# Kernel tuning notes

Measured on AMD Instinct MI355X. Metric: run time of the kernel, lower is better.

Reference implementation:

```python
import jax, jax.numpy as jnp
import numpy as np

H = 1024      # hidden_dim
NH = 16       # num_heads
HD = H // NH  # head_dim
FF = 4096     # ff_dim
EPS = 1e-6


def layer_norm(x, gamma, beta):
    # faithful to source: unbiased std (ddof=1), divide by (std + eps)
    mean = jnp.mean(x, axis=-1, keepdims=True)
    var = jnp.sum((x - mean) ** 2, axis=-1, keepdims=True) / (x.shape[-1] - 1)
    std = jnp.sqrt(var)
    return gamma * (x - mean) / (std + EPS) + beta


def linear_mulbias(x, W, b):
    # source LinearLayer: einsum('...i,io,o->...o') -> (x @ W) * b (bias MULTIPLIES)
    return jnp.einsum('bti,io->bto', x, W) * b


def setup_inputs() -> dict:
    key = jax.random.key(0)
    ks = jax.random.split(key, 11)
    B, T = 2, 2048
    return {
        'x':      jax.random.normal(ks[0], (B, T, H), jnp.float32),
        'Wqkv':   jax.random.normal(ks[1], (H, 3 * H), jnp.float32),
        'bqkv':   jax.random.normal(ks[2], (3 * H,), jnp.float32),
        'W1':     jax.random.normal(ks[3], (H, FF), jnp.float32),
        'b1':     jax.random.normal(ks[4], (FF,), jnp.float32),
        'W2':     jax.random.normal(ks[5], (FF, H), jnp.float32),
        'b2':     jax.random.normal(ks[6], (H,), jnp.float32),
        'gamma1': jax.random.normal(ks[7], (H,), jnp.float32),
        'beta1':  jax.random.normal(ks[8], (H,), jnp.float32),
        'gamma2': jax.random.normal(ks[9], (H,), jnp.float32),
        'beta2':  jax.random.normal(ks[10], (H,), jnp.float32),
    }


def attention(x, Wqkv, bqkv):
    B, T, _ = x.shape
    qkv = linear_mulbias(x, Wqkv, bqkv)                 # [B,T,3H]
    # einops 'b t (d k h) -> k b h t d' with k=3, h=NH: last dim decomposes (d,3,h)
    qkv = qkv.reshape(B, T, HD, 3, NH)
    qkv = jnp.transpose(qkv, (3, 0, 4, 1, 2))           # [3,B,NH,T,HD]
    q, k, v = qkv[0], qkv[1], qkv[2]
    scores = jnp.einsum('bhid,bhjd->bhij', q, k) / (H ** 0.5)  # scale by full hidden_dim
    attn = jax.nn.softmax(scores, axis=-1)
    out = jnp.einsum('bhij,bhjd->bhid', attn, v)        # [B,NH,T,HD]
    return jnp.transpose(out, (0, 2, 1, 3)).reshape(B, T, H)


def reference(x, Wqkv, bqkv, W1, b1, W2, b2, gamma1, beta1, gamma2, beta2):
    # dropout is identity in eval mode
    out = layer_norm(x + attention(x, Wqkv, bqkv), gamma1, beta1)
    ffn = linear_mulbias(jnp.maximum(linear_mulbias(out, W1, b1), 0.0), W2, b2)
    out = layer_norm(out + ffn, gamma2, beta2)
    return out
```

## Files before the change

### kernel.cpp

```cpp
#include <hip/hip_runtime.h>
#include <math.h>

#define B 2
#define T 2048
#define H 1024
#define NH 16
#define HD 64
#define FF 4096
#define M_TOK (B*T)
#define LOG2E 1.4426950408889634f

typedef unsigned short u16;
typedef __attribute__((ext_vector_type(8))) short bf16x8;
typedef __attribute__((ext_vector_type(4))) float f32x4;

#define WAITBAR3  asm volatile("s_waitcnt vmcnt(3)\n\ts_barrier" ::: "memory")
#define WAITBAR4  asm volatile("s_waitcnt vmcnt(4)\n\ts_barrier" ::: "memory")
#define WAITBAR0  asm volatile("s_waitcnt vmcnt(0)\n\ts_barrier" ::: "memory")

__device__ __forceinline__ u16 f2bf(float f) {
  union { float f; unsigned u; } v; v.f = f;
  const unsigned r = (v.u + 0x7FFFu + ((v.u >> 16) & 1u)) >> 16;
  return (u16)r;
}
__device__ __forceinline__ float bf2f(u16 h) {
  union { unsigned u; float f; } v; v.u = ((unsigned)h) << 16;
  return v.f;
}
__device__ __forceinline__ unsigned cvt_pk_bf16(float lo, float hi) {
  unsigned r;
  asm("v_cvt_pk_bf16_f32 %0, %1, %2" : "=v"(r) : "v"(lo), "v"(hi));
  return r;
}
__device__ __forceinline__ float m3(float a, float b, float c) {
  return fmaxf(fmaxf(a, b), c);
}
__device__ __forceinline__ void gload16(const u16* g, u16* l) {
  __builtin_amdgcn_global_load_lds(
      (const __attribute__((address_space(1))) unsigned int*)g,
      (__attribute__((address_space(3))) unsigned int*)l, 16, 0, 0);
}

__global__ __launch_bounds__(256) void preprocess(
    const float* __restrict__ x, u16* __restrict__ xh, u16* __restrict__ xl,
    const float* __restrict__ Wqkv, u16* __restrict__ WqTh, u16* __restrict__ WqTl,
    const float* __restrict__ W1_, u16* __restrict__ W1T_,
    const float* __restrict__ W2_, u16* __restrict__ W2T_)
{
  const int bid = blockIdx.x;
  const int tid = threadIdx.x;
  if (bid < 4096) {
    const size_t i = ((size_t)bid * 256 + tid) * 4;
    const float4 v = *(const float4*)(x + i);
    union { u16 s[4]; uint2 u; } h, l;
    const float f[4] = {v.x, v.y, v.z, v.w};
#pragma unroll
    for (int j = 0; j < 4; ++j) {
      const u16 hb = f2bf(f[j]); h.s[j] = hb; l.s[j] = f2bf(f[j] - bf2f(hb));
    }
    *(uint2*)(xh + i) = h.u;
    *(uint2*)(xl + i) = l.u;
    return;
  }
  __shared__ float tile[64][69];
  const float* in; u16* oh; u16* ol = nullptr; int K, N, k0, n0, split = 0;
  if (bid < 4864) {
    const int tb = bid - 4096;
    in = Wqkv; oh = WqTh; ol = WqTl; K = H; N = 3*H; split = 1;
    n0 = (tb % 48) * 64; k0 = (tb / 48) * 64;
  } else if (bid < 5888) {
    const int tb = bid - 4864;
    in = W1_; oh = W1T_; K = H; N = FF;
    n0 = (tb & 63) * 64; k0 = (tb >> 6) * 64;
  } else {
    const int tb = bid - 5888;
    in = W2_; oh = W2T_; K = FF; N = H;
    n0 = (tb & 15) * 64; k0 = (tb >> 4) * 64;
  }
  const int r = tid >> 4, c4 = (tid & 15) * 4;
#pragma unroll
  for (int i = 0; i < 4; ++i) {
    const float4 v = *(const float4*)(in + (size_t)(k0 + i*16 + r) * N + n0 + c4);
    tile[i*16+r][c4]   = v.x; tile[i*16+r][c4+1] = v.y;
    tile[i*16+r][c4+2] = v.z; tile[i*16+r][c4+3] = v.w;
  }
  __syncthreads();
  const int n = tid >> 2, kq = tid & 3;
  union { u16 s[8]; int4 v; } ph0, ph1, pl0, pl1;
#pragma unroll
  for (int j = 0; j < 8; ++j) {
    const float f0 = tile[kq*16 + j][n];
    const float f1 = tile[kq*16 + 8 + j][n];
    const u16 h0 = f2bf(f0), h1 = f2bf(f1);
    ph0.s[j] = h0; ph1.s[j] = h1;
    if (split) { pl0.s[j] = f2bf(f0 - bf2f(h0)); pl1.s[j] = f2bf(f1 - bf2f(h1)); }
  }
  u16* po = oh + (size_t)(n0 + n) * K + k0 + kq * 16;
  *(int4*)po = ph0.v; *(int4*)(po + 8) = ph1.v;
  if (split) {
    u16* pl = ol + (size_t)(n0 + n) * K + k0 + kq * 16;
    *(int4*)pl = pl0.v; *(int4*)(pl + 8) = pl1.v;
  }
}

__device__ __forceinline__ int swz(int r, int kq) {
  return r * 32 + ((kq ^ ((r >> 1) & 3)) * 8);
}

template<int SPLIT, int RELU, int OBF, int QKV3, int DEEP3>
__global__ __launch_bounds__(256) void mfma_gemm(
    const u16* __restrict__ Ah, const u16* __restrict__ Al,
    const u16* __restrict__ Bh, const u16* __restrict__ Bl,
    const float* __restrict__ bias,
    float* __restrict__ Cf, u16* __restrict__ Cb,
    int M, int N, int K)
{
  __shared__ u16 lds[DEEP3 ? 24576 : (SPLIT ? 32768 : 16384)];
  const int BUFSZ = SPLIT ? 16384 : 8192;
  const int tid = threadIdx.x;
  const int bid = blockIdx.x;
  const int xcd = bid & 7;
  const int idx = bid >> 3;
  const int row0 = (xcd * 4 + (idx & 3)) * 128;
  const int col0 = (idx >> 2) * 128;
  const int wv = tid >> 6, lane = tid & 63;
  const int wr = wv >> 1, wc = wv & 1;
  const int kq = lane >> 4, fr = lane & 15;

  f32x4 acc[4][4] = {};

#define GSTAGE(lbase, gb, rowbase, kk) do { \
    _Pragma("unroll") \
    for (int t_ = 0; t_ < 2; ++t_) { \
      const int c_ = wv * 2 + t_; \
      const int idx_ = c_ * 64 + lane; \
      const int r_ = idx_ >> 2; \
      const int kq_ = (idx_ & 3) ^ ((r_ >> 1) & 3); \
      gload16((gb) + (size_t)((rowbase) + r_) * K + (kk) + kq_ * 8, \
              &lds[(lbase) + c_ * 512]); \
    } } while (0)

#define BLSTAGE(lbase, kk) do { \
    _Pragma("unroll") \
    for (int t_ = 0; t_ < 2; ++t_) { \
      const int c_ = wv * 2 + t_; \
      if (!QKV3 || ((((col0 >> 4) + c_) % 3) != 2)) { \
        const int idx_ = c_ * 64 + lane; \
        const int r_ = idx_ >> 2; \
        const int kq_ = (idx_ & 3) ^ ((r_ >> 1) & 3); \
        gload16(Bl + (size_t)(col0 + r_) * K + (kk) + kq_ * 8, \
                &lds[(lbase) + c_ * 512]); \
      } } } while (0)

  if (DEEP3) {
    const int nk = K >> 5;
    GSTAGE(0, Ah, row0, 0);            GSTAGE(4096, Bh, col0, 0);
    GSTAGE(8192, Ah, row0, 32);        GSTAGE(8192 + 4096, Bh, col0, 32);
    WAITBAR4;
    int cslot = 0, islot = 2;
    for (int i = 0; i < nk; ++i) {
      if (i + 2 < nk) {
        const int kk = (i + 2) * 32;
        GSTAGE(islot * 8192, Ah, row0, kk);
        GSTAGE(islot * 8192 + 4096, Bh, col0, kk);
        islot = (islot == 2) ? 0 : islot + 1;
      }
      const int rb = cslot * 8192;
      bf16x8 a_h[4];
#pragma unroll
      for (int m = 0; m < 4; ++m)
        a_h[m] = *(const bf16x8*)&lds[rb + swz(wr*64 + m*16 + fr, kq)];
#pragma unroll
      for (int n = 0; n < 4; ++n) {
        const bf16x8 b_h = *(const bf16x8*)&lds[rb + 4096 + swz(wc*64 + n*16 + fr, kq)];
#pragma unroll
        for (int m = 0; m < 4; ++m)
          acc[m][n] = __builtin_amdgcn_mfma_f32_16x16x32_bf16(a_h[m], b_h, acc[m][n], 0, 0, 0);
      }
      cslot = (cslot == 2) ? 0 : cslot + 1;
      if (i + 1 < nk) { if (i + 2 < nk) WAITBAR4; else WAITBAR0; }
    }
  } else {
    GSTAGE(0, Ah, row0, 0);
    GSTAGE(4096, Bh, col0, 0);
    if (SPLIT) { GSTAGE(8192, Al, row0, 0); BLSTAGE(12288, 0); }
    __syncthreads();

    int cur = 0;
    for (int k0 = 0; k0 < K; k0 += 32) {
      const int nxt = cur ^ 1;
      if (k0 + 32 < K) {
        GSTAGE(nxt*BUFSZ, Ah, row0, k0 + 32);
        GSTAGE(nxt*BUFSZ + 4096, Bh, col0, k0 + 32);
        if (SPLIT) { GSTAGE(nxt*BUFSZ + 8192, Al, row0, k0 + 32);
                     BLSTAGE(nxt*BUFSZ + 12288, k0 + 32); }
      }
      const int rb = cur * BUFSZ;
      bf16x8 a_h[4], a_l[4];
#pragma unroll
      for (int m = 0; m < 4; ++m) {
        a_h[m] = *(const bf16x8*)&lds[rb + swz(wr*64 + m*16 + fr, kq)];
        if (SPLIT) a_l[m] = *(const bf16x8*)&lds[rb + 8192 + swz(wr*64 + m*16 + fr, kq)];
      }
#pragma unroll
      for (int n = 0; n < 4; ++n) {
        const bf16x8 b_h = *(const bf16x8*)&lds[rb + 4096 + swz(wc*64 + n*16 + fr, kq)];
#pragma unroll
        for (int m = 0; m < 4; ++m)
          acc[m][n] = __builtin_amdgcn_mfma_f32_16x16x32_bf16(a_h[m], b_h, acc[m][n], 0, 0, 0);
        if (SPLIT) {
          const bool dolo = !QKV3 || ((((col0 >> 4) + wc * 4 + n) % 3) != 2);
          if (dolo) {
            const bf16x8 b_l = *(const bf16x8*)&lds[rb + 12288 + swz(wc*64 + n*16 + fr, kq)];
#pragma unroll
            for (int m = 0; m < 4; ++m) {
              acc[m][n] = __builtin_amdgcn_mfma_f32_16x16x32_bf16(a_h[m], b_l, acc[m][n], 0, 0, 0);
              acc[m][n] = __builtin_amdgcn_mfma_f32_16x16x32_bf16(a_l[m], b_h, acc[m][n], 0, 0, 0);
            }
          }
        }
      }
      __syncthreads();
      cur = nxt;
    }
  }
#undef GSTAGE
#undef BLSTAGE

  const int orow0 = row0 + wr * 64, ocol0 = col0 + wc * 64;
#pragma unroll
  for (int n = 0; n < 4; ++n) {
    const int col = ocol0 + n * 16 + fr;
    const float bs = bias[col];
#pragma unroll
    for (int m = 0; m < 4; ++m) {
      const int rbase = orow0 + m * 16 + (lane >> 4) * 4;
#pragma unroll
      for (int j = 0; j < 4; ++j) {
        float v = acc[m][n][j] * bs;
        if (RELU) v = fmaxf(v, 0.0f);
        const size_t off = (size_t)(rbase + j) * N + col;
        if (OBF) Cb[off] = f2bf(v); else Cf[off] = v;
      }
    }
  }
}

__global__ __launch_bounds__(512, 2) void mfma_ffn2(
    const u16* __restrict__ Ah, const u16* __restrict__ Bh,
    const u16* __restrict__ Res, const float* __restrict__ bias,
    float* __restrict__ Y)
{
  const int N = H, K = FF;
  __shared__ u16 lds[2 * 24576];
  const int tid = threadIdx.x;
  const int bid = blockIdx.x;
  const int xcd = bid & 7;
  const int idx = bid >> 3;
  const int row0 = (xcd * 4 + (idx & 3)) * 128;
  const int col0 = (idx >> 2) * 128;
  const int wv8 = tid >> 6, lane = tid & 63;
  const int grp = wv8 >> 2, wv = wv8 & 3;
  const int wr = wv >> 1, wc = wv & 1;
  const int kq = lane >> 4, fr = lane & 15;
  const int kb = grp * (K >> 1);
  u16* gl = &lds[grp * 24576];

  f32x4 acc[4][4] = {};

#define GSTAGE2(lbase, gb, rowbase, kk) do { \
    _Pragma("unroll") \
    for (int t_ = 0; t_ < 2; ++t_) { \
      const int c_ = wv * 2 + t_; \
      const int idx_ = c_ * 64 + lane; \
      const int r_ = idx_ >> 2; \
      const int kq_ = (idx_ & 3) ^ ((r_ >> 1) & 3); \
      gload16((gb) + (size_t)((rowbase) + r_) * K + (kk) + kq_ * 8, \
              &gl[(lbase) + c_ * 512]); \
    } } while (0)

  const int nk = (K >> 1) >> 5;
  GSTAGE2(0, Ah, row0, kb);            GSTAGE2(4096, Bh, col0, kb);
  GSTAGE2(8192, Ah, row0, kb + 32);    GSTAGE2(8192 + 4096, Bh, col0, kb + 32);
  WAITBAR4;
  int cslot = 0, islot = 2;
  for (int i = 0; i < nk; ++i) {
    if (i + 2 < nk) {
      const int kk = kb + (i + 2) * 32;
      GSTAGE2(islot * 8192, Ah, row0, kk);
      GSTAGE2(islot * 8192 + 4096, Bh, col0, kk);
      islot = (islot == 2) ? 0 : islot + 1;
    }
    const int rb = cslot * 8192;
    bf16x8 a_h[4];
#pragma unroll
    for (int m = 0; m < 4; ++m)
      a_h[m] = *(const bf16x8*)&gl[rb + swz(wr*64 + m*16 + fr, kq)];
#pragma unroll
    for (int n = 0; n < 4; ++n) {
      const bf16x8 b_h = *(const bf16x8*)&gl[rb + 4096 + swz(wc*64 + n*16 + fr, kq)];
#pragma unroll
      for (int m = 0; m < 4; ++m)
        acc[m][n] = __builtin_amdgcn_mfma_f32_16x16x32_bf16(a_h[m], b_h, acc[m][n], 0, 0, 0);
    }
    cslot = (cslot == 2) ? 0 : cslot + 1;
    if (i + 1 < nk) { if (i + 2 < nk) WAITBAR4; else WAITBAR0; }
  }
#undef GSTAGE2

  __syncthreads();
  float* fm = (float*)lds;
  const int base = wv * 4096;
  if (grp == 1) {
#pragma unroll
    for (int m = 0; m < 4; ++m)
#pragma unroll
      for (int n = 0; n < 4; ++n)
        *(f32x4*)&fm[base + (m*4 + n)*256 + lane*4] = acc[m][n];
  }
  __syncthreads();
  if (grp == 0) {
    const int orow0 = row0 + wr * 64, ocol0 = col0 + wc * 64;
#pragma unroll
    for (int n = 0; n < 4; ++n) {
      const int col = ocol0 + n * 16 + fr;
      const float bs = bias[col];
#pragma unroll
      for (int m = 0; m < 4; ++m) {
        const f32x4 ob = *(const f32x4*)&fm[base + (m*4 + n)*256 + lane*4];
        const int rbase = orow0 + m * 16 + kq * 4;
#pragma unroll
        for (int j = 0; j < 4; ++j) {
          const size_t off = (size_t)(rbase + j) * N + col;
          Y[off] = bf2f(Res[off]) + (acc[m][n][j] + ob[j]) * bs;
        }
      }
    }
  }
}

__device__ __forceinline__ int padi(int o) { return o + 4 * (o >> 6); }

__global__ __launch_bounds__(256) void repack_qkv(
    const float* __restrict__ qkv,
    u16* __restrict__ Qh, u16* __restrict__ Ql,
    u16* __restrict__ Kh, u16* __restrict__ Kl, u16* __restrict__ Vb)
{
  const int bt = blockIdx.x;
  const int b = bt >> 11, t = bt & (T - 1);
  const int tid = threadIdx.x;
  __shared__ float Ls[3 * H + 192];
  const float* src = qkv + (size_t)bt * (3 * H);
#pragma unroll
  for (int i = 0; i < 3; ++i) {
    const int o = (i * 256 + tid) * 4;
    *(float4*)&Ls[padi(o)] = *(const float4*)(src + o);
  }
  __syncthreads();
  const float qscale = LOG2E / 32.0f;
  const int h = tid >> 4, d0 = (tid & 15) * 4;
  const size_t dst = (((size_t)(b * NH + h)) * T + t) * HD + d0;
  union { u16 s[4]; uint2 u; } qh_, ql_, kh_, kl_, vb_;
#pragma unroll
  for (int jj = 0; jj < 4; ++jj) {
    const int ob = (d0 + jj) * 48 + h;
    const float q = Ls[padi(ob)] * qscale;
    const float k = Ls[padi(ob + 16)];
    const float v = Ls[padi(ob + 32)];
    const u16 qhb = f2bf(q);
    qh_.s[jj] = qhb; ql_.s[jj] = f2bf(q - bf2f(qhb));
    const u16 khb = f2bf(k);
    kh_.s[jj] = khb; kl_.s[jj] = f2bf(k - bf2f(khb));
    vb_.s[jj] = f2bf(v);
  }
  *(uint2*)(Qh + dst) = qh_.u;
  *(uint2*)(Ql + dst) = ql_.u;
  *(uint2*)(Kh + dst) = kh_.u;
  *(uint2*)(Kl + dst) = kl_.u;
  *(uint2*)(Vb + dst) = vb_.u;
}

__global__ __launch_bounds__(256) void vtrans(
    const u16* __restrict__ Vb, u16* __restrict__ VT)
{
  __shared__ u16 Ls[64][72];
  const int bh = blockIdx.y, t0 = blockIdx.x * 64;
  const int tid = threadIdx.x;
  const int r = tid >> 2, c = (tid & 3) * 16;
  const size_t src = ((size_t)bh * T + t0 + r) * HD + c;
  *(int4*)&Ls[r][c]     = *(const int4*)(Vb + src);
  *(int4*)&Ls[r][c + 8] = *(const int4*)(Vb + src + 8);
  __syncthreads();
  const int d = tid >> 2, tc = (tid & 3) * 16;
  u16 buf[16];
#pragma unroll
  for (int i = 0; i < 16; ++i) buf[i] = Ls[tc + i][d];
  u16* dst = VT + ((size_t)bh * HD + d) * T + t0 + tc;
  *(int4*)dst       = *(int4*)&buf[0];
  *(int4*)(dst + 8) = *(int4*)&buf[8];
}

__device__ __forceinline__ int sigma_k(int r) {
  return ((r >> 5) << 5) | (((r >> 2) & 3) << 3) | (((r >> 4) & 1) << 2) | (r & 3);
}

__global__ __launch_bounds__(512, 4) void flash_attn_mfma(
    const u16* __restrict__ Qh, const u16* __restrict__ Ql,
    const u16* __restrict__ Kh, const u16* __restrict__ Kl,
    const u16* __restrict__ VT, float* __restrict__ Out)
{
  __shared__ u16 sm[3 * 12288];
  const int i = blockIdx.x;
  const int slot = i >> 3;
  const int bh = (i & 7) * 4 + (slot >> 4);
  const int row0 = (slot & 15) * 128;
  const int b = bh >> 4, h = bh & 15;
  const int tid = threadIdx.x, wave = tid >> 6, lane = tid & 63;
  const int fr = lane & 15, kq = lane >> 4;

  bf16x8 qh[2], ql[2];
  const size_t qoff = ((size_t)bh * T + row0 + wave*16 + fr) * HD + kq*8;
#pragma unroll
  for (int ks = 0; ks < 2; ++ks) {
    qh[ks] = *(const bf16x8*)(Qh + qoff + ks*32);
    ql[ks] = *(const bf16x8*)(Ql + qoff + ks*32);
  }

  bf16x8 ones8;
#pragma unroll
  for (int z = 0; z < 8; ++z) ones8[z] = (short)0x3F80;

  f32x4 o[4] = {};
  f32x4 oex = {};
  float m_ = -1e30f;

  const int c_ = wave;
  const int r0_ = c_ * 8 + (lane >> 3), s_ = lane & 7;
  const int cd0 = s_ ^ (r0_ & 7);
  const int k0_ = sigma_k(r0_);
  const u16* pKh0 = Kh + ((size_t)bh*T + k0_)*HD + cd0*8;
  const u16* pKl0 = Kl + ((size_t)bh*T + k0_)*HD + cd0*8;
  const u16* pV0  = VT + ((size_t)bh*HD + r0_)*T + cd0*8;

#define FSTAGE(sb) do { \
    gload16(pKh0, &sm[(sb) + c_*512]); \
    gload16(pKl0, &sm[(sb) + 4096 + c_*512]); \
    gload16(pV0,  &sm[(sb) + 8192 + c_*512]); \
    pKh0 += 64*HD; pKl0 += 64*HD; pV0 += 64; \
  } while (0)

  FSTAGE(0);
  FSTAGE(12288);
  WAITBAR3;
  int cslot = 0, islot = 2;

  const int NT = T / 64;
  for (int t = 0; t < NT; ++t) {
    if (t + 2 < NT) {
      FSTAGE(islot * 12288);
      islot = (islot == 2) ? 0 : islot + 1;
    }
    const u16* smb = &sm[cslot * 12288];

    f32x4 s[4] = {};
    __builtin_amdgcn_s_setprio(1);
#pragma unroll
    for (int ks = 0; ks < 2; ++ks) {
#pragma unroll
      for (int n = 0; n < 4; ++n) {
        const int kr = n * 16 + fr;
        const int sl = ((ks*4 + kq) ^ (kr & 7)) * 8;
        const bf16x8 kh_ = *(const bf16x8*)&smb[kr*64 + sl];
        const bf16x8 kl_ = *(const bf16x8*)&smb[4096 + kr*64 + sl];
        s[n] = __builtin_amdgcn_mfma_f32_16x16x32_bf16(kh_, qh[ks], s[n], 0, 0, 0);
        s[n] = __builtin_amdgcn_mfma_f32_16x16x32_bf16(kl_, qh[ks], s[n], 0, 0, 0);
        s[n] = __builtin_amdgcn_mfma_f32_16x16x32_bf16(kh_, ql[ks], s[n], 0, 0, 0);
      }
    }
    __builtin_amdgcn_s_setprio(0);

    const float g0 = m3(s[0][0], s[0][1], s[0][2]);
    const float g1 = m3(s[0][3], s[1][0], s[1][1]);
    const float g2 = m3(s[1][2], s[1][3], s[2][0]);
    const float g3 = m3(s[2][1], s[2][2], s[2][3]);
    const float g4 = m3(s[3][0], s[3][1], s[3][2]);
    float mx = fmaxf(m3(g0, g1, g2), m3(g3, g4, s[3][3]));
    mx = fmaxf(mx, __shfl_xor(mx, 16));
    mx = fmaxf(mx, __shfl_xor(mx, 32));
    if (!__all(mx <= m_ + 8.0f)) {
      const float mn = fmaxf(m_, mx);
      const float fsc = exp2f(m_ - mn);
      m_ = mn;
#pragma unroll
      for (int n = 0; n < 4; ++n) {
        o[n][0] *= fsc; o[n][1] *= fsc;
        o[n][2] *= fsc; o[n][3] *= fsc;
      }
      oex[0] *= fsc; oex[1] *= fsc; oex[2] *= fsc; oex[3] *= fsc;
    }

    float p[4][4];
#pragma unroll
    for (int n = 0; n < 4; ++n)
#pragma unroll
      for (int jj = 0; jj < 4; ++jj)
        p[n][jj] = exp2f(s[n][jj] - m_);

    unsigned pk[4][2];
#pragma unroll
    for (int n = 0; n < 4; ++n) {
      pk[n][0] = cvt_pk_bf16(p[n][0], p[n][1]);
      pk[n][1] = cvt_pk_bf16(p[n][2], p[n][3]);
    }

    __builtin_amdgcn_s_setprio(1);
#pragma unroll
    for (int ks = 0; ks < 2; ++ks) {
      union { unsigned u[4]; bf16x8 v; } pb;
      pb.u[0] = pk[2*ks][0];   pb.u[1] = pk[2*ks][1];
      pb.u[2] = pk[2*ks+1][0]; pb.u[3] = pk[2*ks+1][1];
#pragma unroll
      for (int n = 0; n < 4; ++n) {
        const int dr = n * 16 + fr;
        const bf16x8 vf = *(const bf16x8*)&smb[8192 + dr*64 + (((ks*4 + kq) ^ (dr & 7)) * 8)];
        o[n] = __builtin_amdgcn_mfma_f32_16x16x32_bf16(vf, pb.v, o[n], 0, 0, 0);
      }
      oex = __builtin_amdgcn_mfma_f32_16x16x32_bf16(ones8, pb.v, oex, 0, 0, 0);
    }
    __builtin_amdgcn_s_setprio(0);

    cslot = (cslot == 2) ? 0 : cslot + 1;
    if (t + 1 < NT) { if (t + 2 < NT) WAITBAR3; else WAITBAR0; }
  }
#undef FSTAGE

  {
    const float inv = 1.0f / oex[0];
    const size_t qrow = (size_t)b * T + row0 + wave*16 + fr;
#pragma unroll
    for (int n = 0; n < 4; ++n) {
      float4 ov;
      ov.x = o[n][0] * inv; ov.y = o[n][1] * inv;
      ov.z = o[n][2] * inv; ov.w = o[n][3] * inv;
      *(float4*)(Out + qrow * H + h * HD + n * 16 + kq * 4) = ov;
    }
  }
}

__global__ __launch_bounds__(256) void ln_residual(
    const float* __restrict__ A, const float* __restrict__ Bz,
    const float* __restrict__ gamma, const float* __restrict__ beta,
    u16* __restrict__ obf)
{
  const int row = blockIdx.x, tid = threadIdx.x;
  const int wave = tid >> 6, lane = tid & 63;
  const size_t off = (size_t)row * H + tid * 4;
  const float4 av = *(const float4*)(A + off);
  const float4 bv = *(const float4*)(Bz + off);
  float4 y; y.x = av.x + bv.x; y.y = av.y + bv.y; y.z = av.z + bv.z; y.w = av.w + bv.w;
  float s  = y.x + y.y + y.z + y.w;
  float ss = y.x*y.x + y.y*y.y + y.z*y.z + y.w*y.w;
#pragma unroll
  for (int o = 32; o >= 1; o >>= 1) { s += __shfl_xor(s, o); ss += __shfl_xor(ss, o); }
  __shared__ float red[2][4];
  if (lane == 0) { red[0][wave] = s; red[1][wave] = ss; }
  __syncthreads();
  s  = red[0][0] + red[0][1] + red[0][2] + red[0][3];
  ss = red[1][0] + red[1][1] + red[1][2] + red[1][3];
  const float mean = s * (1.0f / (float)H);
  float var = (ss - (float)H * mean * mean) * (1.0f / (float)(H - 1));
  var = fmaxf(var, 0.0f);
  const float inv = 1.0f / (sqrtf(var) + 1e-6f);
  const float4 gv = *(const float4*)(gamma + tid * 4);
  const float4 be = *(const float4*)(beta + tid * 4);
  float4 o;
  o.x = gv.x * (y.x - mean) * inv + be.x;
  o.y = gv.y * (y.y - mean) * inv + be.y;
  o.z = gv.z * (y.z - mean) * inv + be.z;
  o.w = gv.w * (y.w - mean) * inv + be.w;
  union { u16 s[4]; uint2 u; } pk;
  pk.s[0] = f2bf(o.x); pk.s[1] = f2bf(o.y); pk.s[2] = f2bf(o.z); pk.s[3] = f2bf(o.w);
  *(uint2*)(obf + off) = pk.u;
}

__global__ __launch_bounds__(256) void ln_only(
    const float* __restrict__ Yv,
    const float* __restrict__ gamma, const float* __restrict__ beta,
    float* __restrict__ out)
{
  const int row = blockIdx.x, tid = threadIdx.x;
  const int wave = tid >> 6, lane = tid & 63;
  const size_t off = (size_t)row * H + tid * 4;
  const float4 y = *(const float4*)(Yv + off);
  float s  = y.x + y.y + y.z + y.w;
  float ss = y.x*y.x + y.y*y.y + y.z*y.z + y.w*y.w;
#pragma unroll
  for (int o = 32; o >= 1; o >>= 1) { s += __shfl_xor(s, o); ss += __shfl_xor(ss, o); }
  __shared__ float red[2][4];
  if (lane == 0) { red[0][wave] = s; red[1][wave] = ss; }
  __syncthreads();
  s  = red[0][0] + red[0][1] + red[0][2] + red[0][3];
  ss = red[1][0] + red[1][1] + red[1][2] + red[1][3];
  const float mean = s * (1.0f / (float)H);
  float var = (ss - (float)H * mean * mean) * (1.0f / (float)(H - 1));
  var = fmaxf(var, 0.0f);
  const float inv = 1.0f / (sqrtf(var) + 1e-6f);
  const float4 gv = *(const float4*)(gamma + tid * 4);
  const float4 be = *(const float4*)(beta + tid * 4);
  float4 o;
  o.x = gv.x * (y.x - mean) * inv + be.x;
  o.y = gv.y * (y.y - mean) * inv + be.y;
  o.z = gv.z * (y.z - mean) * inv + be.z;
  o.w = gv.w * (y.w - mean) * inv + be.w;
  *(float4*)(out + off) = o;
}

extern "C" void kernel_launch(void* const* d_in, const int* in_sizes, int n_in,
                              void* d_out, int out_size, void* d_ws, size_t ws_size,
                              hipStream_t stream)
{
  const float* x    = (const float*)d_in[0];
  const float* Wqkv = (const float*)d_in[1];
  const float* bqkv = (const float*)d_in[2];
  const float* W1   = (const float*)d_in[3];
  const float* b1   = (const float*)d_in[4];
  const float* W2   = (const float*)d_in[5];
  const float* b2   = (const float*)d_in[6];
  const float* g1   = (const float*)d_in[7];
  const float* be1  = (const float*)d_in[8];
  const float* g2   = (const float*)d_in[9];
  const float* be2  = (const float*)d_in[10];
  float* out = (float*)d_out;
  char* w = (char*)d_ws;

  float* qkv  = (float*)(w + 0);
  u16*   h1b  = (u16*)  (w + 0);
  u16*   xh   = (u16*)  (w + 52428800);
  u16*   xl   = (u16*)  (w + 60817408);
  u16*   Qh   = (u16*)  (w + 52428800);
  u16*   Ql   = (u16*)  (w + 60817408);
  u16*   WqTh = (u16*)  (w + 69206016);
  u16*   WqTl = (u16*)  (w + 75497472);
  u16*   Khb  = (u16*)  (w + 69206016);
  u16*   Klb  = (u16*)  (w + 77594624);
  u16*   Vbb  = (u16*)  (w + 85983232);
  u16*   VTb  = (u16*)  (w + 94371840);
  float* attn = (float*)(w + 102760448);
  float* Yb   = (float*)(w + 102760448);
  u16*   W1T  = (u16*)  (w + 119537664);
  u16*   W2T  = (u16*)  (w + 127926272);
  u16*   ln1b = (u16*)  (w + 136314880);

  preprocess<<<6912, 256, 0, stream>>>(x, xh, xl, Wqkv, WqTh, WqTl,
                                       W1, W1T, W2, W2T);
  mfma_gemm<1,0,0,1,0><<<24 * 32, 256, 0, stream>>>(xh, xl, WqTh, WqTl, bqkv,
                                                    qkv, nullptr, M_TOK, 3*H, H);
  repack_qkv<<<M_TOK, 256, 0, stream>>>(qkv, Qh, Ql, Khb, Klb, Vbb);
  vtrans<<<dim3(T/64, B*NH), 256, 0, stream>>>(Vbb, VTb);
  flash_attn_mfma<<<512, 512, 0, stream>>>(Qh, Ql, Khb, Klb, VTb, attn);
  ln_residual<<<M_TOK, 256, 0, stream>>>(x, attn, g1, be1, ln1b);
  mfma_gemm<0,1,1,0,1><<<32 * 32, 256, 0, stream>>>(ln1b, nullptr, W1T, nullptr, b1,
                                                    nullptr, h1b, M_TOK, FF, H);
  mfma_ffn2<<<256, 512, 0, stream>>>(h1b, W2T, ln1b, b2, Yb);
  ln_only<<<M_TOK, 256, 0, stream>>>(Yb, g2, be2, out);
}
```

Measured before the change: 292.2 us.

## Fuse QKV repack into QKV GEMM epilogue via permuted weight columns

Permutes the Wqkv columns (and the bias) during preprocessing so the QKV GEMM output columns come out grouped as Q, K, V by head and dim. A dedicated QKV GEMM kernel then writes bf16 hi/lo Q, K and V directly in head-major layout, which removes the fp32 qkv intermediate and the separate repack kernel. It also picks the split-precision path per block (V blocks skip the low parts) instead of per fragment. The epilogue writes are scattered 2-byte stores, which could be less efficient than the old coalesced repack.

After: 268.3 us. 8.2% less time.

```diff
diff --git a/kernel.cpp b/kernel.cpp
--- a/kernel.cpp
+++ b/kernel.cpp
@@ -41,14 +41,29 @@
       (__attribute__((address_space(3))) unsigned int*)l, 16, 0, 0);
 }
 
+__device__ __forceinline__ int colperm(int c) {
+  const int d = c / 48;
+  const int rem = c - d * 48;
+  return ((rem >> 4) << 10) | ((rem & 15) << 6) | d;
+}
+
 __global__ __launch_bounds__(256) void preprocess(
     const float* __restrict__ x, u16* __restrict__ xh, u16* __restrict__ xl,
     const float* __restrict__ Wqkv, u16* __restrict__ WqTh, u16* __restrict__ WqTl,
     const float* __restrict__ W1_, u16* __restrict__ W1T_,
-    const float* __restrict__ W2_, u16* __restrict__ W2T_)
+    const float* __restrict__ W2_, u16* __restrict__ W2T_,
+    const float* __restrict__ bqkv, float* __restrict__ bqkvP)
 {
   const int bid = blockIdx.x;
   const int tid = threadIdx.x;
+  if (bid == 6912) {
+#pragma unroll
+    for (int it = 0; it < 12; ++it) {
+      const int c = it * 256 + tid;
+      bqkvP[colperm(c)] = bqkv[c];
+    }
+    return;
+  }
   if (bid < 4096) {
     const size_t i = ((size_t)bid * 256 + tid) * 4;
     const float4 v = *(const float4*)(x + i);
@@ -63,10 +78,11 @@
     return;
   }
   __shared__ float tile[64][69];
-  const float* in; u16* oh; u16* ol = nullptr; int K, N, k0, n0, split = 0;
+  const float* in; u16* oh; u16* ol = nullptr;
+  int K, N, k0, n0, split = 0, permq = 0;
   if (bid < 4864) {
     const int tb = bid - 4096;
-    in = Wqkv; oh = WqTh; ol = WqTl; K = H; N = 3*H; split = 1;
+    in = Wqkv; oh = WqTh; ol = WqTl; K = H; N = 3*H; split = 1; permq = 1;
     n0 = (tb % 48) * 64; k0 = (tb / 48) * 64;
   } else if (bid < 5888) {
     const int tb = bid - 4864;
@@ -95,10 +111,12 @@
     ph0.s[j] = h0; ph1.s[j] = h1;
     if (split) { pl0.s[j] = f2bf(f0 - bf2f(h0)); pl1.s[j] = f2bf(f1 - bf2f(h1)); }
   }
-  u16* po = oh + (size_t)(n0 + n) * K + k0 + kq * 16;
+  int orow = n0 + n;
+  if (permq) orow = colperm(orow);
+  u16* po = oh + (size_t)orow * K + k0 + kq * 16;
   *(int4*)po = ph0.v; *(int4*)(po + 8) = ph1.v;
   if (split) {
-    u16* pl = ol + (size_t)(n0 + n) * K + k0 + kq * 16;
+    u16* pl = ol + (size_t)orow * K + k0 + kq * 16;
     *(int4*)pl = pl0.v; *(int4*)(pl + 8) = pl1.v;
   }
 }
@@ -107,16 +125,14 @@
   return r * 32 + ((kq ^ ((r >> 1) & 3)) * 8);
 }
 
-template<int SPLIT, int RELU, int OBF, int QKV3, int DEEP3>
+template<int RELU, int OBF>
 __global__ __launch_bounds__(256) void mfma_gemm(
-    const u16* __restrict__ Ah, const u16* __restrict__ Al,
-    const u16* __restrict__ Bh, const u16* __restrict__ Bl,
+    const u16* __restrict__ Ah, const u16* __restrict__ Bh,
     const float* __restrict__ bias,
     float* __restrict__ Cf, u16* __restrict__ Cb,
     int M, int N, int K)
 {
-  __shared__ u16 lds[DEEP3 ? 24576 : (SPLIT ? 32768 : 16384)];
-  const int BUFSZ = SPLIT ? 16384 : 8192;
+  __shared__ u16 lds[24576];
   const int tid = threadIdx.x;
   const int bid = blockIdx.x;
   const int xcd = bid & 7;
@@ -140,92 +156,34 @@
               &lds[(lbase) + c_ * 512]); \
     } } while (0)
 
-#define BLSTAGE(lbase, kk) do { \
-    _Pragma("unroll") \
-    for (int t_ = 0; t_ < 2; ++t_) { \
-      const int c_ = wv * 2 + t_; \
-      if (!QKV3 || ((((col0 >> 4) + c_) % 3) != 2)) { \
-        const int idx_ = c_ * 64 + lane; \
-        const int r_ = idx_ >> 2; \
-        const int kq_ = (idx_ & 3) ^ ((r_ >> 1) & 3); \
-        gload16(Bl + (size_t)(col0 + r_) * K + (kk) + kq_ * 8, \
-                &lds[(lbase) + c_ * 512]); \
-      } } } while (0)
-
-  if (DEEP3) {
-    const int nk = K >> 5;
-    GSTAGE(0, Ah, row0, 0);            GSTAGE(4096, Bh, col0, 0);
-    GSTAGE(8192, Ah, row0, 32);        GSTAGE(8192 + 4096, Bh, col0, 32);
-    WAITBAR4;
-    int cslot = 0, islot = 2;
-    for (int i = 0; i < nk; ++i) {
-      if (i + 2 < nk) {
-        const int kk = (i + 2) * 32;
-        GSTAGE(islot * 8192, Ah, row0, kk);
-        GSTAGE(islot * 8192 + 4096, Bh, col0, kk);
-        islot = (islot == 2) ? 0 : islot + 1;
-      }
-      const int rb = cslot * 8192;
-      bf16x8 a_h[4];
+  const int nk = K >> 5;
+  GSTAGE(0, Ah, row0, 0);            GSTAGE(4096, Bh, col0, 0);
+  GSTAGE(8192, Ah, row0, 32);        GSTAGE(8192 + 4096, Bh, col0, 32);
+  WAITBAR4;
+  int cslot = 0, islot = 2;
+  for (int i = 0; i < nk; ++i) {
+    if (i + 2 < nk) {
+      const int kk = (i + 2) * 32;
+      GSTAGE(islot * 8192, Ah, row0, kk);
+      GSTAGE(islot * 8192 + 4096, Bh, col0, kk);
+      islot = (islot == 2) ? 0 : islot + 1;
+    }
+    const int rb = cslot * 8192;
+    bf16x8 a_h[4];
+#pragma unroll
+    for (int m = 0; m < 4; ++m)
+      a_h[m] = *(const bf16x8*)&lds[rb + swz(wr*64 + m*16 + fr, kq)];
+#pragma unroll
+    for (int n = 0; n < 4; ++n) {
+      const bf16x8 b_h = *(const bf16x8*)&lds[rb + 4096 + swz(wc*64 + n*16 + fr, kq)];
 #pragma unroll
       for (int m = 0; m < 4; ++m)
-        a_h[m] = *(const bf16x8*)&lds[rb + swz(wr*64 + m*16 + fr, kq)];
-#pragma unroll
-      for (int n = 0; n < 4; ++n) {
-        const bf16x8 b_h = *(const bf16x8*)&lds[rb + 4096 + swz(wc*64 + n*16 + fr, kq)];
-#pragma unroll
-        for (int m = 0; m < 4; ++m)
-          acc[m][n] = __builtin_amdgcn_mfma_f32_16x16x32_bf16(a_h[m], b_h, acc[m][n], 0, 0, 0);
-      }
-      cslot = (cslot == 2) ? 0 : cslot + 1;
-      if (i + 1 < nk) { if (i + 2 < nk) WAITBAR4; else WAITBAR0; }
-    }
-  } else {
-    GSTAGE(0, Ah, row0, 0);
-    GSTAGE(4096, Bh, col0, 0);
-    if (SPLIT) { GSTAGE(8192, Al, row0, 0); BLSTAGE(12288, 0); }
-    __syncthreads();
-
-    int cur = 0;
-    for (int k0 = 0; k0 < K; k0 += 32) {
-      const int nxt = cur ^ 1;
-      if (k0 + 32 < K) {
-        GSTAGE(nxt*BUFSZ, Ah, row0, k0 + 32);
-        GSTAGE(nxt*BUFSZ + 4096, Bh, col0, k0 + 32);
-        if (SPLIT) { GSTAGE(nxt*BUFSZ + 8192, Al, row0, k0 + 32);
-                     BLSTAGE(nxt*BUFSZ + 12288, k0 + 32); }
-      }
-      const int rb = cur * BUFSZ;
-      bf16x8 a_h[4], a_l[4];
-#pragma unroll
-      for (int m = 0; m < 4; ++m) {
-        a_h[m] = *(const bf16x8*)&lds[rb + swz(wr*64 + m*16 + fr, kq)];
-        if (SPLIT) a_l[m] = *(const bf16x8*)&lds[rb + 8192 + swz(wr*64 + m*16 + fr, kq)];
-      }
-#pragma unroll
-      for (int n = 0; n < 4; ++n) {
-        const bf16x8 b_h = *(const bf16x8*)&lds[rb + 4096 + swz(wc*64 + n*16 + fr, kq)];
-#pragma unroll
-        for (int m = 0; m < 4; ++m)
-          acc[m][n] = __builtin_amdgcn_mfma_f32_16x16x32_bf16(a_h[m], b_h, acc[m][n], 0, 0, 0);
-        if (SPLIT) {
-          const bool dolo = !QKV3 || ((((col0 >> 4) + wc * 4 + n) % 3) != 2);
-          if (dolo) {
-            const bf16x8 b_l = *(const bf16x8*)&lds[rb + 12288 + swz(wc*64 + n*16 + fr, kq)];
-#pragma unroll
-            for (int m = 0; m < 4; ++m) {
-              acc[m][n] = __builtin_amdgcn_mfma_f32_16x16x32_bf16(a_h[m], b_l, acc[m][n], 0, 0, 0);
-              acc[m][n] = __builtin_amdgcn_mfma_f32_16x16x32_bf16(a_l[m], b_h, acc[m][n], 0, 0, 0);
-            }
-          }
-        }
-      }
-      __syncthreads();
-      cur = nxt;
-    }
+        acc[m][n] = __builtin_amdgcn_mfma_f32_16x16x32_bf16(a_h[m], b_h, acc[m][n], 0, 0, 0);
+    }
+    cslot = (cslot == 2) ? 0 : cslot + 1;
+    if (i + 1 < nk) { if (i + 2 < nk) WAITBAR4; else WAITBAR0; }
   }
 #undef GSTAGE
-#undef BLSTAGE
 
   const int orow0 = row0 + wr * 64, ocol0 = col0 + wc * 64;
 #pragma unroll
@@ -234,13 +192,119 @@
     const float bs = bias[col];
 #pragma unroll
     for (int m = 0; m < 4; ++m) {
-      const int rbase = orow0 + m * 16 + (lane >> 4) * 4;
+      const int rbase = orow0 + m * 16 + kq * 4;
 #pragma unroll
       for (int j = 0; j < 4; ++j) {
         float v = acc[m][n][j] * bs;
         if (RELU) v = fmaxf(v, 0.0f);
         const size_t off = (size_t)(rbase + j) * N + col;
         if (OBF) Cb[off] = f2bf(v); else Cf[off] = v;
+      }
+    }
+  }
+}
+
+__global__ __launch_bounds__(256) void mfma_qkv(
+    const u16* __restrict__ Ah, const u16* __restrict__ Al,
+    const u16* __restrict__ Bh, const u16* __restrict__ Bl,
+    const float* __restrict__ biasP,
+    u16* __restrict__ Qh, u16* __restrict__ Ql,
+    u16* __restrict__ Kh, u16* __restrict__ Kl, u16* __restrict__ Vb)
+{
+  const int K = H;
+  __shared__ u16 lds[32768];
+  const int tid = threadIdx.x;
+  const int bid = blockIdx.x;
+  const int xcd = bid & 7;
+  const int idx = bid >> 3;
+  const int row0 = (xcd * 4 + (idx & 3)) * 128;
+  const int col0 = (idx >> 2) * 128;
+  const int wv = tid >> 6, lane = tid & 63;
+  const int wr = wv >> 1, wc = wv & 1;
+  const int kq = lane >> 4, fr = lane & 15;
+  const bool isV = (col0 >= 2048);
+
+  f32x4 acc[4][4] = {};
+
+#define QSTAGE(lbase, gb, rowbase, kk) do { \
+    _Pragma("unroll") \
+    for (int t_ = 0; t_ < 2; ++t_) { \
+      const int c_ = wv * 2 + t_; \
+      const int idx_ = c_ * 64 + lane; \
+      const int r_ = idx_ >> 2; \
+      const int kq_ = (idx_ & 3) ^ ((r_ >> 1) & 3); \
+      gload16((gb) + (size_t)((rowbase) + r_) * K + (kk) + kq_ * 8, \
+              &lds[(lbase) + c_ * 512]); \
+    } } while (0)
+
+  QSTAGE(0, Ah, row0, 0);
+  QSTAGE(4096, Bh, col0, 0);
+  if (!isV) { QSTAGE(8192, Al, row0, 0); QSTAGE(12288, Bl, col0, 0); }
+  __syncthreads();
+
+  int cur = 0;
+  for (int k0 = 0; k0 < K; k0 += 32) {
+    const int nxt = cur ^ 1;
+    if (k0 + 32 < K) {
+      QSTAGE(nxt*16384, Ah, row0, k0 + 32);
+      QSTAGE(nxt*16384 + 4096, Bh, col0, k0 + 32);
+      if (!isV) { QSTAGE(nxt*16384 + 8192, Al, row0, k0 + 32);
+                  QSTAGE(nxt*16384 + 12288, Bl, col0, k0 + 32); }
+    }
+    const int rb = cur * 16384;
+    bf16x8 a_h[4], a_l[4];
+#pragma unroll
+    for (int m = 0; m < 4; ++m) {
+      a_h[m] = *(const bf16x8*)&lds[rb + swz(wr*64 + m*16 + fr, kq)];
+      if (!isV) a_l[m] = *(const bf16x8*)&lds[rb + 8192 + swz(wr*64 + m*16 + fr, kq)];
+    }
+#pragma unroll
+    for (int n = 0; n < 4; ++n) {
+      const bf16x8 b_h = *(const bf16x8*)&lds[rb + 4096 + swz(wc*64 + n*16 + fr, kq)];
+#pragma unroll
+      for (int m = 0; m < 4; ++m)
+        acc[m][n] = __builtin_amdgcn_mfma_f32_16x16x32_bf16(a_h[m], b_h, acc[m][n], 0, 0, 0);
+      if (!isV) {
+        const bf16x8 b_l = *(const bf16x8*)&lds[rb + 12288 + swz(wc*64 + n*16 + fr, kq)];
+#pragma unroll
+        for (int m = 0; m < 4; ++m) {
+          acc[m][n] = __builtin_amdgcn_mfma_f32_16x16x32_bf16(a_h[m], b_l, acc[m][n], 0, 0, 0);
+          acc[m][n] = __builtin_amdgcn_mfma_f32_16x16x32_bf16(a_l[m], b_h, acc[m][n], 0, 0, 0);
+        }
+      }
+    }
+    __syncthreads();
+    cur = nxt;
+  }
+#undef QSTAGE
+
+  const float qscale = LOG2E / 32.0f;
+  const int orow0 = row0 + wr * 64, ocol0 = col0 + wc * 64;
+  const int kcls = col0 >> 10;
+#pragma unroll
+  for (int n = 0; n < 4; ++n) {
+    const int colp = ocol0 + n * 16 + fr;
+    const int d = colp & 63, hh = (colp >> 6) & 15;
+    const float bs = biasP[colp];
+#pragma unroll
+    for (int m = 0; m < 4; ++m) {
+      const int rbase = orow0 + m * 16 + kq * 4;
+#pragma unroll
+      for (int j = 0; j < 4; ++j) {
+        const int row = rbase + j;
+        const int b = row >> 11, t = row & (T - 1);
+        const size_t dst = (((size_t)(b * NH + hh)) * T + t) * HD + d;
+        float v = acc[m][n][j] * bs;
+        if (kcls == 0) {
+          v *= qscale;
+          const u16 hb = f2bf(v);
+          Qh[dst] = hb; Ql[dst] = f2bf(v - bf2f(hb));
+        } else if (kcls == 1) {
+          const u16 hb = f2bf(v);
+          Kh[dst] = hb; Kl[dst] = f2bf(v - bf2f(hb));
+        } else {
+          Vb[dst] = f2bf(v);
+        }
       }
     }
   }
@@ -337,47 +401,6 @@
       }
     }
   }
-}
-
-__device__ __forceinline__ int padi(int o) { return o + 4 * (o >> 6); }
-
-__global__ __launch_bounds__(256) void repack_qkv(
-    const float* __restrict__ qkv,
-    u16* __restrict__ Qh, u16* __restrict__ Ql,
-    u16* __restrict__ Kh, u16* __restrict__ Kl, u16* __restrict__ Vb)
-{
-  const int bt = blockIdx.x;
-  const int b = bt >> 11, t = bt & (T - 1);
-  const int tid = threadIdx.x;
-  __shared__ float Ls[3 * H + 192];
-  const float* src = qkv + (size_t)bt * (3 * H);
-#pragma unroll
-  for (int i = 0; i < 3; ++i) {
-    const int o = (i * 256 + tid) * 4;
-    *(float4*)&Ls[padi(o)] = *(const float4*)(src + o);
-  }
-  __syncthreads();
-  const float qscale = LOG2E / 32.0f;
-  const int h = tid >> 4, d0 = (tid & 15) * 4;
-  const size_t dst = (((size_t)(b * NH + h)) * T + t) * HD + d0;
-  union { u16 s[4]; uint2 u; } qh_, ql_, kh_, kl_, vb_;
-#pragma unroll
-  for (int jj = 0; jj < 4; ++jj) {
-    const int ob = (d0 + jj) * 48 + h;
-    const float q = Ls[padi(ob)] * qscale;
-    const float k = Ls[padi(ob + 16)];
-    const float v = Ls[padi(ob + 32)];
-    const u16 qhb = f2bf(q);
-    qh_.s[jj] = qhb; ql_.s[jj] = f2bf(q - bf2f(qhb));
-    const u16 khb = f2bf(k);
-    kh_.s[jj] = khb; kl_.s[jj] = f2bf(k - bf2f(khb));
-    vb_.s[jj] = f2bf(v);
-  }
-  *(uint2*)(Qh + dst) = qh_.u;
-  *(uint2*)(Ql + dst) = ql_.u;
-  *(uint2*)(Kh + dst) = kh_.u;
-  *(uint2*)(Kl + dst) = kl_.u;
-  *(uint2*)(Vb + dst) = vb_.u;
 }
 
 __global__ __launch_bounds__(256) void vtrans(
@@ -633,34 +656,33 @@
   float* out = (float*)d_out;
   char* w = (char*)d_ws;
 
-  float* qkv  = (float*)(w + 0);
-  u16*   h1b  = (u16*)  (w + 0);
-  u16*   xh   = (u16*)  (w + 52428800);
-  u16*   xl   = (u16*)  (w + 60817408);
-  u16*   Qh   = (u16*)  (w + 52428800);
-  u16*   Ql   = (u16*)  (w + 60817408);
-  u16*   WqTh = (u16*)  (w + 69206016);
-  u16*   WqTl = (u16*)  (w + 75497472);
-  u16*   Khb  = (u16*)  (w + 69206016);
-  u16*   Klb  = (u16*)  (w + 77594624);
-  u16*   Vbb  = (u16*)  (w + 85983232);
-  u16*   VTb  = (u16*)  (w + 94371840);
-  float* attn = (float*)(w + 102760448);
-  float* Yb   = (float*)(w + 102760448);
-  u16*   W1T  = (u16*)  (w + 119537664);
-  u16*   W2T  = (u16*)  (w + 127926272);
-  u16*   ln1b = (u16*)  (w + 136314880);
-
-  preprocess<<<6912, 256, 0, stream>>>(x, xh, xl, Wqkv, WqTh, WqTl,
-                                       W1, W1T, W2, W2T);
-  mfma_gemm<1,0,0,1,0><<<24 * 32, 256, 0, stream>>>(xh, xl, WqTh, WqTl, bqkv,
-                                                    qkv, nullptr, M_TOK, 3*H, H);
-  repack_qkv<<<M_TOK, 256, 0, stream>>>(qkv, Qh, Ql, Khb, Klb, Vbb);
+  u16*   Qh    = (u16*)  (w + 0);
+  u16*   Ql    = (u16*)  (w + 8388608);
+  u16*   Khb   = (u16*)  (w + 16777216);
+  u16*   Klb   = (u16*)  (w + 25165824);
+  u16*   Vbb   = (u16*)  (w + 33554432);
+  u16*   VTb   = (u16*)  (w + 41943040);
+  u16*   h1b   = (u16*)  (w + 0);
+  u16*   xh    = (u16*)  (w + 52428800);
+  u16*   xl    = (u16*)  (w + 60817408);
+  u16*   WqTh  = (u16*)  (w + 69206016);
+  u16*   WqTl  = (u16*)  (w + 75497472);
+  float* attn  = (float*)(w + 102760448);
+  float* Yb    = (float*)(w + 102760448);
+  u16*   W1T   = (u16*)  (w + 119537664);
+  u16*   W2T   = (u16*)  (w + 127926272);
+  u16*   ln1b  = (u16*)  (w + 136314880);
+  float* bqkvP = (float*)(w + 144703488);
+
+  preprocess<<<6913, 256, 0, stream>>>(x, xh, xl, Wqkv, WqTh, WqTl,
+                                       W1, W1T, W2, W2T, bqkv, bqkvP);
+  mfma_qkv<<<24 * 32, 256, 0, stream>>>(xh, xl, WqTh, WqTl, bqkvP,
+                                        Qh, Ql, Khb, Klb, Vbb);
   vtrans<<<dim3(T/64, B*NH), 256, 0, stream>>>(Vbb, VTb);
   flash_attn_mfma<<<512, 512, 0, stream>>>(Qh, Ql, Khb, Klb, VTb, attn);
   ln_residual<<<M_TOK, 256, 0, stream>>>(x, attn, g1, be1, ln1b);
-  mfma_gemm<0,1,1,0,1><<<32 * 32, 256, 0, stream>>>(ln1b, nullptr, W1T, nullptr, b1,
-                                                    nullptr, h1b, M_TOK, FF, H);
+  mfma_gemm<1,1><<<32 * 32, 256, 0, stream>>>(ln1b, W1T, b1,
+                                              nullptr, h1b, M_TOK, FF, H);
   mfma_ffn2<<<256, 512, 0, stream>>>(h1b, W2T, ln1b, b2, Yb);
   ln_only<<<M_TOK, 256, 0, stream>>>(Yb, g2, be2, out);
 }
```
